# Kernel optimization log

Hardware: AMD Instinct MI355X
Metric: run time of the kernel (lower is better)

The kernel has to match this reference:

```python
import jax, jax.numpy as jnp
import numpy as np

N, E, IN, H, D = 100000, 1600000, 128, 4, 64
NEG_SLOPE = 0.2
K_APPNP, ALPHA = 5, 0.5
BN_EPS = 1e-5


def setup_inputs() -> dict:
    key = jax.random.key(0)
    ks = jax.random.split(key, 12)
    return {
        'node_feats': jax.random.normal(ks[0], (N, IN), jnp.float32),
        'src': jax.random.randint(ks[1], (E,), 0, N, jnp.int32),
        'dst': jax.random.randint(ks[2], (E,), 0, N, jnp.int32),
        'W_fc': jax.random.normal(ks[3], (IN, H * D), jnp.float32) * (1.0 / np.sqrt(IN)),
        'attn_l': jax.random.normal(ks[4], (H, D), jnp.float32) * 0.1,
        'attn_r': jax.random.normal(ks[5], (H, D), jnp.float32) * 0.1,
        'W_res_gat': jax.random.normal(ks[6], (IN, H * D), jnp.float32) * (1.0 / np.sqrt(IN)),
        'gat_bias': jax.random.normal(ks[7], (H * D,), jnp.float32) * 0.01,
        'conv_w': jax.random.normal(ks[8], (1, H), jnp.float32) * 0.5,
        'conv_b': jax.random.normal(ks[9], (1,), jnp.float32) * 0.01,
        'W_res': jax.random.normal(ks[10], (D, IN), jnp.float32) * (1.0 / np.sqrt(IN)),
        'b_res': jax.random.normal(ks[11], (D,), jnp.float32) * 0.01,
        'gamma': jnp.ones((D,), jnp.float32),
        'beta': jnp.zeros((D,), jnp.float32),
    }


def reference(node_feats, src, dst, W_fc, attn_l, attn_r, W_res_gat, gat_bias,
              conv_w, conv_b, W_res, b_res, gamma, beta):
    # ---- GATConv (4 heads, residual, relu) ----
    feat = (node_feats @ W_fc).reshape(N, H, D)            # (N,H,D)
    el = jnp.einsum('nhd,hd->nh', feat, attn_l)            # (N,H)
    er = jnp.einsum('nhd,hd->nh', feat, attn_r)
    e = jax.nn.leaky_relu(el[src] + er[dst], NEG_SLOPE)    # (E,H)
    # edge softmax over incoming edges of each dst node
    emax = jax.ops.segment_max(e, dst, num_segments=N)     # (N,H)
    emax = jnp.where(jnp.isfinite(emax), emax, 0.0)
    ee = jnp.exp(e - emax[dst])                            # (E,H)
    denom = jax.ops.segment_sum(ee, dst, num_segments=N)   # (N,H)
    a = ee / jnp.maximum(denom[dst], 1e-9)                 # (E,H)
    msg = feat[src] * a[..., None]                         # (E,H,D)
    rst = jax.ops.segment_sum(msg, dst, num_segments=N)    # (N,H,D)
    resval = (node_feats @ W_res_gat).reshape(N, H, D)
    rst = jax.nn.relu(rst + resval + gat_bias.reshape(1, H, D))
    # ---- Conv1d (heads -> 1, kernel_size=1) then flatten ----
    h = jnp.einsum('nhd,oh->nod', rst, conv_w) + conv_b[None, :, None]
    h = h.reshape(N, D)
    # ---- APPNP (k=5, alpha=0.5), symmetric deg^{-1/2} norm (in-degree, clamp 1) ----
    deg = jax.ops.segment_sum(jnp.ones((E,), jnp.float32), dst, num_segments=N)
    norm = jnp.power(jnp.maximum(deg, 1.0), -0.5)[:, None]  # (N,1)
    h0 = h
    for _ in range(K_APPNP):
        h = jax.ops.segment_sum((h * norm)[src], dst, num_segments=N) * norm
        h = (1.0 - ALPHA) * h + ALPHA * h0
    # ---- residual linear + relu ----
    h = h + jax.nn.relu(node_feats @ W_res.T + b_res)
    # ---- BatchNorm1d (batch stats, affine) ----
    mu = h.mean(axis=0)
    var = h.var(axis=0)
    return (h - mu) * jax.lax.rsqrt(var + BN_EPS) * gamma + beta
```

## Files before the change

kernel.cpp:

```cpp
#include <hip/hip_runtime.h>
#include <math.h>

#define NN 100000
#define NE 1600000
#define NEG_SLOPE 0.2f

typedef __attribute__((ext_vector_type(8))) short bf16x8;
typedef __attribute__((ext_vector_type(4))) float f32x4;
typedef __attribute__((ext_vector_type(2))) float f32x2;

__device__ __forceinline__ float b2f(unsigned short u) {
  union { unsigned u; float f; } c; c.u = ((unsigned)u) << 16; return c.f;
}
__device__ __forceinline__ unsigned short f2b(float x) {
  union { float f; unsigned u; } c; c.f = x;
  unsigned r = c.u + 0x7FFFu + ((c.u >> 16) & 1u);
  return (unsigned short)(r >> 16);
}
__device__ __forceinline__ void fma4(float4& acc, float s, const float4& b) {
  acc.x = fmaf(s, b.x, acc.x);
  acc.y = fmaf(s, b.y, acc.y);
  acc.z = fmaf(s, b.z, acc.z);
  acc.w = fmaf(s, b.w, acc.w);
}
__device__ __forceinline__ float wred(float v) {
#pragma unroll
  for (int off = 32; off > 0; off >>= 1) v += __shfl_xor(v, off, 64);
  return v;
}

__global__ __launch_bounds__(256) void k_zero(int* __restrict__ p, int nwords) {
  int i = blockIdx.x * 256 + threadIdx.x;
  if (i < nwords) p[i] = 0;
}

__global__ void k_zrow(unsigned short* __restrict__ a, unsigned short* __restrict__ b) {
  int i = threadIdx.x;
  a[(size_t)NN * 64 + i] = 0;
  b[(size_t)NN * 64 + i] = 0;
}

__global__ __launch_bounds__(256) void k_cast(const float* __restrict__ A, unsigned short* __restrict__ Ab) {
  int i = blockIdx.x * 256 + threadIdx.x;
  int i4 = i * 4;
  if (i4 < NN * 128) {
    float4 v = *(const float4*)&A[i4];
    ushort4 o; o.x = f2b(v.x); o.y = f2b(v.y); o.z = f2b(v.z); o.w = f2b(v.w);
    *(ushort4*)&Ab[i4] = o;
  }
}

__global__ __launch_bounds__(256) void k_deg(const int* __restrict__ dst, int* __restrict__ deg) {
  int i = blockIdx.x * 256 + threadIdx.x;
  if (i < NE) atomicAdd(&deg[dst[i]], 1);
}

__global__ __launch_bounds__(256) void k_alloc(const int* __restrict__ deg, int* __restrict__ row_start,
                                               int* __restrict__ counter, float* __restrict__ nrm) {
  int i = blockIdx.x * 256 + threadIdx.x;
  if (i < NN) {
    row_start[i] = atomicAdd(counter, deg[i]);
    nrm[i] = rsqrtf(fmaxf((float)deg[i], 1.0f));
  }
}

__global__ __launch_bounds__(256) void k_scatter(const int* __restrict__ src, const int* __restrict__ dst,
                                                 const int* __restrict__ row_start, int* __restrict__ cursor,
                                                 int* __restrict__ csr_src) {
  int i = blockIdx.x * 256 + threadIdx.x;
  if (i < NE) {
    int n = dst[i];
    int p = atomicAdd(&cursor[n], 1);
    csr_src[row_start[n] + p] = src[i];
  }
}

__global__ __launch_bounds__(256) void k_prepw(const float* __restrict__ W_fc, const float* __restrict__ al,
                                               const float* __restrict__ ar, float* __restrict__ w) {
  int o = blockIdx.x * 256 + threadIdx.x;
  if (o >= 1024) return;
  int side = o >> 9;
  int h = (o >> 7) & 3;
  int k = o & 127;
  const float* a = side ? ar : al;
  float s = 0.f;
  for (int d = 0; d < 64; ++d) s += W_fc[k * 256 + h * 64 + d] * a[h * 64 + d];
  w[(side * 4 + h) * 128 + k] = s;
}

__global__ __launch_bounds__(256) void k_elr2(const float* __restrict__ X, const float* __restrict__ w,
                                              float* __restrict__ el, float* __restrict__ er) {
  int n = blockIdx.x * 32 + (threadIdx.x >> 3);
  int p = threadIdx.x & 7;
  if (n >= NN) return;
  const float4* xr = (const float4*)(X + (size_t)n * 128);
  const float4* wr = (const float4*)(w + p * 128);
  float s = 0.f;
#pragma unroll
  for (int i = 0; i < 32; ++i) {
    float4 x = xr[i], ww = wr[i];
    s += x.x * ww.x + x.y * ww.y + x.z * ww.z + x.w * ww.w;
  }
  if (p < 4) el[n * 4 + p] = s;
  else er[n * 4 + (p - 4)] = s;
}

__global__ __launch_bounds__(256) void k_prepB(const float* __restrict__ W_fc, const float* __restrict__ W_rg,
                                               unsigned short* __restrict__ Bp) {
  int y = blockIdx.y;
  const float* Bsrc = (y >> 1) ? W_rg : W_fc;
  int colbase = (y & 1) * 128;
  for (int e = blockIdx.x * 256 + threadIdx.x; e < 16384; e += 2048) {
    int n = e & 127, k = e >> 7;
    int p = colbase + n;
    int d = p >> 2, hh = p & 3;
    float v = Bsrc[k * 256 + hh * 64 + d];
    int nt = n >> 4, nn = n & 15, kt = k >> 5, quad = (k >> 3) & 3, j = k & 7;
    Bp[(size_t)y * 16384 + ((nt * 4 + kt) * 64 + quad * 16 + nn) * 8 + j] = f2b(v);
  }
}

__global__ __launch_bounds__(256) void k_gemm_mfma(const unsigned short* __restrict__ Abf,
                                                   const unsigned short* __restrict__ Bp,
                                                   unsigned* __restrict__ feat8u,
                                                   unsigned short* __restrict__ resval2) {
  __shared__ unsigned short Bl[16384];
  int tid = threadIdx.x;
  int half = blockIdx.y >> 1;
  int colbase = (blockIdx.y & 1) * 128;
  {
    const uint4* src = (const uint4*)(Bp + (size_t)blockIdx.y * 16384);
    uint4* dst4 = (uint4*)Bl;
#pragma unroll
    for (int i = 0; i < 8; ++i) dst4[tid + i * 256] = src[tid + i * 256];
  }
  __syncthreads();
  int w = tid >> 6, lane = tid & 63;
  int quad = lane >> 4;
  int row0 = blockIdx.x * 128;
  int mrow = row0 + (lane & 15);
  f32x4 acc[8][2];
#pragma unroll
  for (int rt = 0; rt < 8; ++rt)
#pragma unroll
    for (int c = 0; c < 2; ++c) acc[rt][c] = (f32x4){0.f, 0.f, 0.f, 0.f};
#pragma unroll
  for (int kt = 0; kt < 4; ++kt) {
    bf16x8 b0 = *(const bf16x8*)&Bl[(((w * 2 + 0) * 4 + kt) * 64 + lane) * 8];
    bf16x8 b1 = *(const bf16x8*)&Bl[(((w * 2 + 1) * 4 + kt) * 64 + lane) * 8];
    int kb = kt * 32 + quad * 8;
#pragma unroll
    for (int rt = 0; rt < 8; ++rt) {
      int rr = mrow + rt * 16; if (rr > NN - 1) rr = NN - 1;
      bf16x8 a = *(const bf16x8*)&Abf[(size_t)rr * 128 + kb];
      acc[rt][0] = __builtin_amdgcn_mfma_f32_16x16x32_bf16(b0, a, acc[rt][0], 0, 0, 0);
      acc[rt][1] = __builtin_amdgcn_mfma_f32_16x16x32_bf16(b1, a, acc[rt][1], 0, 0, 0);
    }
  }
#pragma unroll
  for (int rt = 0; rt < 8; ++rt) {
    int m = row0 + rt * 16 + (lane & 15);
    if (m < NN) {
#pragma unroll
      for (int c = 0; c < 2; ++c) {
        int col = colbase + (w * 2 + c) * 16 + quad * 4;
        if (half == 0) {
          int pk = __builtin_amdgcn_cvt_pk_fp8_f32(acc[rt][c][0], acc[rt][c][1], 0, false);
          pk = __builtin_amdgcn_cvt_pk_fp8_f32(acc[rt][c][2], acc[rt][c][3], pk, true);
          feat8u[(size_t)m * 64 + (col >> 2)] = (unsigned)pk;
        } else {
          ushort4 o;
          o.x = f2b(acc[rt][c][0]); o.y = f2b(acc[rt][c][1]);
          o.z = f2b(acc[rt][c][2]); o.w = f2b(acc[rt][c][3]);
          *(ushort4*)&resval2[(size_t)m * 256 + col] = o;
        }
      }
    }
  }
}

__global__ __launch_bounds__(256) void k_gemm_nt_bias_relu(const float* __restrict__ A, const float* __restrict__ B,
                                                           const float* __restrict__ bias, float* __restrict__ C) {
  __shared__ float Bl[128][68];
  for (int idx = threadIdx.x; idx < 64 * 128; idx += 256) {
    int d = idx >> 7, k = idx & 127;
    Bl[k][d] = B[d * 128 + k];
  }
  __syncthreads();
  int tx = threadIdx.x & 15, ty = threadIdx.x >> 4;
  int row0 = blockIdx.x * 64 + ty * 4;
  const float* ap[4];
#pragma unroll
  for (int r = 0; r < 4; ++r) ap[r] = A + (size_t)min(row0 + r, NN - 1) * 128;
  float4 acc[4];
#pragma unroll
  for (int r = 0; r < 4; ++r) acc[r] = make_float4(0.f, 0.f, 0.f, 0.f);
#pragma unroll 2
  for (int k0 = 0; k0 < 128; k0 += 4) {
    float4 b0 = *(const float4*)&Bl[k0][tx * 4];
    float4 b1 = *(const float4*)&Bl[k0 + 1][tx * 4];
    float4 b2 = *(const float4*)&Bl[k0 + 2][tx * 4];
    float4 b3 = *(const float4*)&Bl[k0 + 3][tx * 4];
#pragma unroll
    for (int r = 0; r < 4; ++r) {
      float4 a = *(const float4*)(ap[r] + k0);
      fma4(acc[r], a.x, b0); fma4(acc[r], a.y, b1);
      fma4(acc[r], a.z, b2); fma4(acc[r], a.w, b3);
    }
  }
  float4 bv = *(const float4*)&bias[tx * 4];
#pragma unroll
  for (int r = 0; r < 4; ++r) {
    int row = row0 + r;
    if (row < NN) {
      float4 v;
      v.x = fmaxf(acc[r].x + bv.x, 0.f);
      v.y = fmaxf(acc[r].y + bv.y, 0.f);
      v.z = fmaxf(acc[r].z + bv.z, 0.f);
      v.w = fmaxf(acc[r].w + bv.w, 0.f);
      *(float4*)&C[(size_t)row * 64 + tx * 4] = v;
    }
  }
}

__global__ __launch_bounds__(256) void k_gat(const int* __restrict__ row_start, const int* __restrict__ deg,
                                             const int* __restrict__ csr_src, const float* __restrict__ el,
                                             const float* __restrict__ er, const unsigned* __restrict__ feat8u,
                                             const unsigned short* __restrict__ resval2,
                                             const float* __restrict__ gat_bias, const float* __restrict__ conv_w,
                                             const float* __restrict__ conv_b, const float* __restrict__ nrm,
                                             float* __restrict__ h0, unsigned short* __restrict__ hsA) {
  __shared__ int s_src[4][64];
  __shared__ float s_x[4][64][4];
  int wid = threadIdx.x >> 6, lane = threadIdx.x & 63;
  int n = blockIdx.x * 4 + wid;
  if (n >= NN) return;
  int s0 = row_start[n], cnt = deg[n];
  float4 er4 = *(const float4*)&er[n * 4];
  int k = lane & 31, g = lane >> 5;
  unsigned koff = (unsigned)(k << 3);
  f32x2 a01_0 = (f32x2){0.f, 0.f}, a23_0 = (f32x2){0.f, 0.f};
  f32x2 a01_1 = (f32x2){0.f, 0.f}, a23_1 = (f32x2){0.f, 0.f};
  float den0 = 0.f, den1 = 0.f, den2 = 0.f, den3 = 0.f;
  for (int base = 0; base < cnt; base += 64) {
    int j = base + lane;
    int s = 0;
    float x0 = 0.f, x1 = 0.f, x2 = 0.f, x3 = 0.f;
    if (j < cnt) {
      s = csr_src[s0 + j];
      float4 el4 = *(const float4*)&el[s * 4];
      float e0 = el4.x + er4.x; e0 = (e0 > 0.f) ? e0 : NEG_SLOPE * e0;
      float e1 = el4.y + er4.y; e1 = (e1 > 0.f) ? e1 : NEG_SLOPE * e1;
      float e2 = el4.z + er4.z; e2 = (e2 > 0.f) ? e2 : NEG_SLOPE * e2;
      float e3 = el4.w + er4.w; e3 = (e3 > 0.f) ? e3 : NEG_SLOPE * e3;
      x0 = __expf(e0); x1 = __expf(e1); x2 = __expf(e2); x3 = __expf(e3);
      den0 += x0; den1 += x1; den2 += x2; den3 += x3;
    }
    s_src[wid][lane] = s;
    *(float4*)&s_x[wid][lane][0] = make_float4(x0, x1, x2, x3);
    int m = cnt - base; if (m > 64) m = 64;
    int mr = (m + 3) & ~3;
    for (int t = 0; t < mr; t += 4) {
      int sA = s_src[wid][t + g];
      int sB = s_src[wid][t + 2 + g];
      float4 xA = *(const float4*)&s_x[wid][t + g][0];
      float4 xB = *(const float4*)&s_x[wid][t + 2 + g][0];
      uint2 fA = *(const uint2*)((const char*)feat8u + (((unsigned)sA << 8) + koff));
      uint2 fB = *(const uint2*)((const char*)feat8u + (((unsigned)sB << 8) + koff));
      f32x2 xa01 = (f32x2){xA.x, xA.y}, xa23 = (f32x2){xA.z, xA.w};
      f32x2 xb01 = (f32x2){xB.x, xB.y}, xb23 = (f32x2){xB.z, xB.w};
      f32x2 lo, hi;
      lo = __builtin_amdgcn_cvt_pk_f32_fp8((int)fA.x, false);
      hi = __builtin_amdgcn_cvt_pk_f32_fp8((int)fA.x, true);
      a01_0 += xa01 * lo; a23_0 += xa23 * hi;
      lo = __builtin_amdgcn_cvt_pk_f32_fp8((int)fA.y, false);
      hi = __builtin_amdgcn_cvt_pk_f32_fp8((int)fA.y, true);
      a01_1 += xa01 * lo; a23_1 += xa23 * hi;
      lo = __builtin_amdgcn_cvt_pk_f32_fp8((int)fB.x, false);
      hi = __builtin_amdgcn_cvt_pk_f32_fp8((int)fB.x, true);
      a01_0 += xb01 * lo; a23_0 += xb23 * hi;
      lo = __builtin_amdgcn_cvt_pk_f32_fp8((int)fB.y, false);
      hi = __builtin_amdgcn_cvt_pk_f32_fp8((int)fB.y, true);
      a01_1 += xb01 * lo; a23_1 += xb23 * hi;
    }
  }
  den0 = wred(den0); den1 = wred(den1); den2 = wred(den2); den3 = wred(den3);
  float i0 = 1.f / fmaxf(den0, 1e-9f);
  float i1 = 1.f / fmaxf(den1, 1e-9f);
  float i2 = 1.f / fmaxf(den2, 1e-9f);
  float i3 = 1.f / fmaxf(den3, 1e-9f);
  a01_0[0] += __shfl_xor(a01_0[0], 32, 64);
  a01_0[1] += __shfl_xor(a01_0[1], 32, 64);
  a23_0[0] += __shfl_xor(a23_0[0], 32, 64);
  a23_0[1] += __shfl_xor(a23_0[1], 32, 64);
  a01_1[0] += __shfl_xor(a01_1[0], 32, 64);
  a01_1[1] += __shfl_xor(a01_1[1], 32, 64);
  a23_1[0] += __shfl_xor(a23_1[0], 32, 64);
  a23_1[1] += __shfl_xor(a23_1[1], 32, 64);
  if (lane < 32) {
    int d0 = k << 1;
    uint4 rv = *(const uint4*)&resval2[(size_t)n * 256 + ((unsigned)k << 3)];
    float2 bb0 = *(const float2*)&gat_bias[d0];
    float2 bb1 = *(const float2*)&gat_bias[64 + d0];
    float2 bb2 = *(const float2*)&gat_bias[128 + d0];
    float2 bb3 = *(const float2*)&gat_bias[192 + d0];
    float cb = conv_b[0];
    float cw0 = conv_w[0], cw1 = conv_w[1], cw2 = conv_w[2], cw3 = conv_w[3];
    float t, hm0 = cb, hm1 = cb;
    t = fmaf(a01_0[0], i0, b2f((unsigned short)(rv.x & 0xffffu)) + bb0.x); t = fmaxf(t, 0.f); hm0 = fmaf(cw0, t, hm0);
    t = fmaf(a01_0[1], i1, b2f((unsigned short)(rv.x >> 16)) + bb1.x);     t = fmaxf(t, 0.f); hm0 = fmaf(cw1, t, hm0);
    t = fmaf(a23_0[0], i2, b2f((unsigned short)(rv.y & 0xffffu)) + bb2.x); t = fmaxf(t, 0.f); hm0 = fmaf(cw2, t, hm0);
    t = fmaf(a23_0[1], i3, b2f((unsigned short)(rv.y >> 16)) + bb3.x);     t = fmaxf(t, 0.f); hm0 = fmaf(cw3, t, hm0);
    t = fmaf(a01_1[0], i0, b2f((unsigned short)(rv.z & 0xffffu)) + bb0.y); t = fmaxf(t, 0.f); hm1 = fmaf(cw0, t, hm1);
    t = fmaf(a01_1[1], i1, b2f((unsigned short)(rv.z >> 16)) + bb1.y);     t = fmaxf(t, 0.f); hm1 = fmaf(cw1, t, hm1);
    t = fmaf(a23_1[0], i2, b2f((unsigned short)(rv.w & 0xffffu)) + bb2.y); t = fmaxf(t, 0.f); hm1 = fmaf(cw2, t, hm1);
    t = fmaf(a23_1[1], i3, b2f((unsigned short)(rv.w >> 16)) + bb3.y);     t = fmaxf(t, 0.f); hm1 = fmaf(cw3, t, hm1);
    float nn_ = nrm[n];
    size_t o = (size_t)n * 64 + d0;
    *(float2*)&h0[o] = make_float2(hm0, hm1);
    ushort2 hs; hs.x = f2b(hm0 * nn_); hs.y = f2b(hm1 * nn_);
    *(ushort2*)&hsA[o] = hs;
  }
}

__device__ __forceinline__ void gather_accum(const int* __restrict__ row_start, const int* __restrict__ deg,
                                             const int* __restrict__ csr_src,
                                             const unsigned short* __restrict__ hs_in,
                                             int n, int wid, int lane,
                                             float& a0, float& a1, float& a2, float& a3) {
  __shared__ int s_src[4][64];
  int s0 = row_start[n], cnt = deg[n];
  int k = lane & 15, g = lane >> 4;
  unsigned koff = (unsigned)(k << 3);
  a0 = 0.f; a1 = 0.f; a2 = 0.f; a3 = 0.f;
  for (int base = 0; base < cnt; base += 64) {
    int j = base + lane;
    s_src[wid][lane] = (j < cnt) ? csr_src[s0 + j] : NN;
    int m = cnt - base; if (m > 64) m = 64;
    int mr = (m + 7) & ~7;
    for (int t = 0; t < mr; t += 8) {
      int sA = s_src[wid][t + g];
      int sB = s_src[wid][t + 4 + g];
      uint2 uA = *(const uint2*)((const char*)hs_in + (((unsigned)sA << 7) + koff));
      uint2 uB = *(const uint2*)((const char*)hs_in + (((unsigned)sB << 7) + koff));
      a0 += __uint_as_float(uA.x << 16);
      a1 += __uint_as_float(uA.x & 0xFFFF0000u);
      a2 += __uint_as_float(uA.y << 16);
      a3 += __uint_as_float(uA.y & 0xFFFF0000u);
      a0 += __uint_as_float(uB.x << 16);
      a1 += __uint_as_float(uB.x & 0xFFFF0000u);
      a2 += __uint_as_float(uB.y << 16);
      a3 += __uint_as_float(uB.y & 0xFFFF0000u);
    }
  }
  a0 += __shfl_xor(a0, 16, 64); a1 += __shfl_xor(a1, 16, 64);
  a2 += __shfl_xor(a2, 16, 64); a3 += __shfl_xor(a3, 16, 64);
  a0 += __shfl_xor(a0, 32, 64); a1 += __shfl_xor(a1, 32, 64);
  a2 += __shfl_xor(a2, 32, 64); a3 += __shfl_xor(a3, 32, 64);
}

__global__ __launch_bounds__(256) void k_gather_mid(const int* __restrict__ row_start, const int* __restrict__ deg,
                                                    const int* __restrict__ csr_src,
                                                    const unsigned short* __restrict__ hs_in,
                                                    const float* __restrict__ nrm, const float* __restrict__ h0,
                                                    unsigned short* __restrict__ hs_out) {
  int wid = threadIdx.x >> 6, lane = threadIdx.x & 63;
  int n = blockIdx.x * 4 + wid;
  if (n >= NN) return;
  float a0, a1, a2, a3;
  gather_accum(row_start, deg, csr_src, hs_in, n, wid, lane, a0, a1, a2, a3);
  if (lane < 16) {
    size_t o = (size_t)n * 64 + (lane << 2);
    float nn_ = nrm[n];
    float4 h4 = *(const float4*)&h0[o];
    float hn = 0.5f * nn_;
    float v0 = fmaf(hn, a0, 0.5f * h4.x) * nn_;
    float v1 = fmaf(hn, a1, 0.5f * h4.y) * nn_;
    float v2 = fmaf(hn, a2, 0.5f * h4.z) * nn_;
    float v3 = fmaf(hn, a3, 0.5f * h4.w) * nn_;
    ushort4 ov; ov.x = f2b(v0); ov.y = f2b(v1); ov.z = f2b(v2); ov.w = f2b(v3);
    *(ushort4*)&hs_out[o] = ov;
  }
}

__global__ __launch_bounds__(256) void k_gather_last(const int* __restrict__ row_start, const int* __restrict__ deg,
                                                     const int* __restrict__ csr_src,
                                                     const unsigned short* __restrict__ hs_in,
                                                     const float* __restrict__ nrm,
                                                     const float* __restrict__ res2,
                                                     float* h0io) {
  int wid = threadIdx.x >> 6, lane = threadIdx.x & 63;
  int n = blockIdx.x * 4 + wid;
  if (n >= NN) return;
  float a0, a1, a2, a3;
  gather_accum(row_start, deg, csr_src, hs_in, n, wid, lane, a0, a1, a2, a3);
  if (lane < 16) {
    size_t o = (size_t)n * 64 + (lane << 2);
    float nn_ = nrm[n];
    float4 h4 = *(const float4*)&h0io[o];
    float4 r4 = *(const float4*)&res2[o];
    float hn = 0.5f * nn_;
    float4 v;
    v.x = fmaf(hn, a0, 0.5f * h4.x) + r4.x;
    v.y = fmaf(hn, a1, 0.5f * h4.y) + r4.y;
    v.z = fmaf(hn, a2, 0.5f * h4.z) + r4.z;
    v.w = fmaf(hn, a3, 0.5f * h4.w) + r4.w;
    *(float4*)&h0io[o] = v;
  }
}

__global__ __launch_bounds__(256) void k_finred(const float* __restrict__ hfin, float* __restrict__ bn) {
  __shared__ float s1[256], s2[256];
  int d = threadIdx.x & 63;
  int rb = blockIdx.x * 64;
  float sum = 0.f, sq = 0.f;
  for (int r = threadIdx.x >> 6; r < 64; r += 4) {
    int n = rb + r;
    if (n < NN) {
      float v = hfin[(size_t)n * 64 + d];
      sum += v; sq += v * v;
    }
  }
  s1[threadIdx.x] = sum; s2[threadIdx.x] = sq;
  __syncthreads();
  if (threadIdx.x < 128) { s1[threadIdx.x] += s1[threadIdx.x + 128]; s2[threadIdx.x] += s2[threadIdx.x + 128]; }
  __syncthreads();
  if (threadIdx.x < 64) {
    atomicAdd(&bn[d], s1[threadIdx.x] + s1[threadIdx.x + 64]);
    atomicAdd(&bn[64 + d], s2[threadIdx.x] + s2[threadIdx.x + 64]);
  }
}

__global__ void k_bnstats(const float* __restrict__ bn, const float* __restrict__ gamma,
                          const float* __restrict__ beta, float* __restrict__ bns) {
  int d = threadIdx.x;
  float mu = bn[d] * (1.0f / NN);
  float var = fmaxf(bn[64 + d] * (1.0f / NN) - mu * mu, 0.f);
  float sc = rsqrtf(var + 1e-5f) * gamma[d];
  bns[d] = sc;
  bns[64 + d] = beta[d] - mu * sc;
}

__global__ __launch_bounds__(256) void k_bnapply(const float* __restrict__ h, const float* __restrict__ bns,
                                                 float* __restrict__ out) {
  int i = blockIdx.x * 256 + threadIdx.x;
  if (i < NN * 64) {
    int d = i & 63;
    out[i] = fmaf(h[i], bns[d], bns[64 + d]);
  }
}

extern "C" void kernel_launch(void* const* d_in, const int* in_sizes, int n_in,
                              void* d_out, int out_size, void* d_ws, size_t ws_size,
                              hipStream_t stream) {
  const float* node_feats = (const float*)d_in[0];
  const int* src = (const int*)d_in[1];
  const int* dst = (const int*)d_in[2];
  const float* W_fc = (const float*)d_in[3];
  const float* attn_l = (const float*)d_in[4];
  const float* attn_r = (const float*)d_in[5];
  const float* W_res_gat = (const float*)d_in[6];
  const float* gat_bias = (const float*)d_in[7];
  const float* conv_w = (const float*)d_in[8];
  const float* conv_b = (const float*)d_in[9];
  const float* W_res = (const float*)d_in[10];
  const float* b_res = (const float*)d_in[11];
  const float* gamma = (const float*)d_in[12];
  const float* beta = (const float*)d_in[13];
  float* out = (float*)d_out;

  char* base = (char*)d_ws;
  size_t off = 0;
  auto alloc = [&](size_t bytes) -> char* {
    char* p = base + off;
    off = (off + bytes + 255) & ~(size_t)255;
    return p;
  };
  unsigned* feat8u        = (unsigned*)alloc((size_t)NN * 256);
  unsigned short* resval2 = (unsigned short*)alloc((size_t)NN * 256 * 2);
  float* res2             = (float*)resval2;
  float* el               = (float*)alloc((size_t)NN * 4 * 4);
  float* er               = (float*)alloc((size_t)NN * 4 * 4);
  float* h0               = (float*)alloc((size_t)NN * 64 * 4);
  unsigned short* Abf     = (unsigned short*)h0;
  unsigned short* hsA     = (unsigned short*)alloc((size_t)(NN + 1) * 64 * 2);
  unsigned short* hsB     = (unsigned short*)alloc((size_t)(NN + 1) * 64 * 2);
  int* csr_src            = (int*)alloc((size_t)NE * 4);
  float* nrm              = (float*)alloc((size_t)NN * 4);
  int* row_start          = (int*)alloc((size_t)NN * 4);
  unsigned short* Bpacked = (unsigned short*)alloc((size_t)4 * 16384 * 2);
  float* w_elr            = (float*)alloc((size_t)8 * 128 * 4);
  size_t zoff = off;
  int* deg                = (int*)alloc((size_t)NN * 4);
  int* cursor             = (int*)alloc((size_t)NN * 4);
  int* counter            = (int*)alloc(256);
  float* bn               = (float*)alloc(256 * 4);
  float* hfin             = h0;

  int zwords = (int)((off - zoff) / 4);
  int gE = (NE + 255) / 256;
  int gN = (NN + 255) / 256;
  int gW = (NN + 3) / 4;
  int gM = (NN + 63) / 64;
  int gV = (NN * 64 + 255) / 256;

  k_zero<<<(zwords + 255) / 256, 256, 0, stream>>>((int*)(base + zoff), zwords);
  k_zrow<<<1, 64, 0, stream>>>(hsA, hsB);
  k_deg<<<gE, 256, 0, stream>>>(dst, deg);
  k_alloc<<<gN, 256, 0, stream>>>(deg, row_start, counter, nrm);
  k_scatter<<<gE, 256, 0, stream>>>(src, dst, row_start, cursor, csr_src);

  k_cast<<<(NN * 128 / 4 + 255) / 256, 256, 0, stream>>>(node_feats, Abf);
  k_prepB<<<dim3(8, 4), 256, 0, stream>>>(W_fc, W_res_gat, Bpacked);
  k_prepw<<<4, 256, 0, stream>>>(W_fc, attn_l, attn_r, w_elr);
  k_gemm_mfma<<<dim3((NN + 127) / 128, 4), 256, 0, stream>>>(Abf, Bpacked, feat8u, resval2);

  k_elr2<<<(NN + 31) / 32, 256, 0, stream>>>(node_feats, w_elr, el, er);
  k_gat<<<gW, 256, 0, stream>>>(row_start, deg, csr_src, el, er, feat8u, resval2,
                                gat_bias, conv_w, conv_b, nrm, h0, hsA);

  k_gemm_nt_bias_relu<<<gM, 256, 0, stream>>>(node_feats, W_res, b_res, res2);

  k_gather_mid<<<gW, 256, 0, stream>>>(row_start, deg, csr_src, hsA, nrm, h0, hsB);
  k_gather_mid<<<gW, 256, 0, stream>>>(row_start, deg, csr_src, hsB, nrm, h0, hsA);
  k_gather_mid<<<gW, 256, 0, stream>>>(row_start, deg, csr_src, hsA, nrm, h0, hsB);
  k_gather_mid<<<gW, 256, 0, stream>>>(row_start, deg, csr_src, hsB, nrm, h0, hsA);
  k_gather_last<<<gW, 256, 0, stream>>>(row_start, deg, csr_src, hsA, nrm, res2, hfin);

  k_finred<<<gM, 256, 0, stream>>>(hfin, bn);
  k_bnstats<<<1, 64, 0, stream>>>(bn, gamma, beta, bn + 128);
  k_bnapply<<<gV, 256, 0, stream>>>(hfin, bn + 128, out);
}
```

Before: 834.9 us.

## Stage GEMM A tile in LDS, coalesce epilogue stores, fuse softmax denominator

The MFMA GEMM now copies the 128x128 bf16 A tile into padded LDS and loads B in two K halves, so the smaller B buffer makes room in LDS. The epilogue writes its results through LDS and then stores full coalesced 16-byte rows to feat8u and resval2, replacing the scattered 4- and 8-byte global writes. In the GAT kernel, the softmax denominator is now accumulated inside the gather loop from the staged values, which replaces the 6-step wave reduction with a single xor-32 shuffle. The cost is more LDS per block, which may lower occupancy, plus extra barriers.

```diff
diff --git a/kernel.cpp b/kernel.cpp
--- a/kernel.cpp
+++ b/kernel.cpp
@@ -22,11 +22,6 @@
   acc.y = fmaf(s, b.y, acc.y);
   acc.z = fmaf(s, b.z, acc.z);
   acc.w = fmaf(s, b.w, acc.w);
-}
-__device__ __forceinline__ float wred(float v) {
-#pragma unroll
-  for (int off = 32; off > 0; off >>= 1) v += __shfl_xor(v, off, 64);
-  return v;
 }
 
 __global__ __launch_bounds__(256) void k_zero(int* __restrict__ p, int nwords) {
@@ -116,7 +111,7 @@
     int d = p >> 2, hh = p & 3;
     float v = Bsrc[k * 256 + hh * 64 + d];
     int nt = n >> 4, nn = n & 15, kt = k >> 5, quad = (k >> 3) & 3, j = k & 7;
-    Bp[(size_t)y * 16384 + ((nt * 4 + kt) * 64 + quad * 16 + nn) * 8 + j] = f2b(v);
+    Bp[(size_t)y * 16384 + ((kt * 8 + nt) * 64 + quad * 16 + nn) * 8 + j] = f2b(v);
   }
 }
 
@@ -124,57 +119,96 @@
                                                    const unsigned short* __restrict__ Bp,
                                                    unsigned* __restrict__ feat8u,
                                                    unsigned short* __restrict__ resval2) {
-  __shared__ unsigned short Bl[16384];
+  __shared__ unsigned short Al[128 * 136];
+  __shared__ unsigned short Bl[8192];
   int tid = threadIdx.x;
   int half = blockIdx.y >> 1;
   int colbase = (blockIdx.y & 1) * 128;
+  int row0 = blockIdx.x * 128;
+#pragma unroll
+  for (int i = 0; i < 8; ++i) {
+    int c = tid + i * 256;
+    int row = c >> 4, part = c & 15;
+    int gr = row0 + row; if (gr > NN - 1) gr = NN - 1;
+    *(uint4*)&Al[row * 136 + part * 8] = *(const uint4*)&Abf[(size_t)gr * 128 + part * 8];
+  }
   {
-    const uint4* src = (const uint4*)(Bp + (size_t)blockIdx.y * 16384);
+    const uint4* srcb = (const uint4*)(Bp + (size_t)blockIdx.y * 16384);
     uint4* dst4 = (uint4*)Bl;
 #pragma unroll
-    for (int i = 0; i < 8; ++i) dst4[tid + i * 256] = src[tid + i * 256];
+    for (int i = 0; i < 4; ++i) dst4[tid + i * 256] = srcb[tid + i * 256];
   }
   __syncthreads();
   int w = tid >> 6, lane = tid & 63;
-  int quad = lane >> 4;
-  int row0 = blockIdx.x * 128;
-  int mrow = row0 + (lane & 15);
+  int quad = lane >> 4, l16 = lane & 15;
   f32x4 acc[8][2];
 #pragma unroll
   for (int rt = 0; rt < 8; ++rt)
 #pragma unroll
     for (int c = 0; c < 2; ++c) acc[rt][c] = (f32x4){0.f, 0.f, 0.f, 0.f};
 #pragma unroll
-  for (int kt = 0; kt < 4; ++kt) {
-    bf16x8 b0 = *(const bf16x8*)&Bl[(((w * 2 + 0) * 4 + kt) * 64 + lane) * 8];
-    bf16x8 b1 = *(const bf16x8*)&Bl[(((w * 2 + 1) * 4 + kt) * 64 + lane) * 8];
-    int kb = kt * 32 + quad * 8;
-#pragma unroll
-    for (int rt = 0; rt < 8; ++rt) {
-      int rr = mrow + rt * 16; if (rr > NN - 1) rr = NN - 1;
-      bf16x8 a = *(const bf16x8*)&Abf[(size_t)rr * 128 + kb];
-      acc[rt][0] = __builtin_amdgcn_mfma_f32_16x16x32_bf16(b0, a, acc[rt][0], 0, 0, 0);
-      acc[rt][1] = __builtin_amdgcn_mfma_f32_16x16x32_bf16(b1, a, acc[rt][1], 0, 0, 0);
-    }
-  }
-#pragma unroll
-  for (int rt = 0; rt < 8; ++rt) {
-    int m = row0 + rt * 16 + (lane & 15);
-    if (m < NN) {
+  for (int kh = 0; kh < 2; ++kh) {
+    if (kh == 1) {
+      __syncthreads();
+      const uint4* srcb = (const uint4*)(Bp + (size_t)blockIdx.y * 16384 + 8192);
+      uint4* dst4 = (uint4*)Bl;
+#pragma unroll
+      for (int i = 0; i < 4; ++i) dst4[tid + i * 256] = srcb[tid + i * 256];
+      __syncthreads();
+    }
+#pragma unroll
+    for (int ktl = 0; ktl < 2; ++ktl) {
+      int kt = kh * 2 + ktl;
+      bf16x8 b0 = *(const bf16x8*)&Bl[((ktl * 8 + w * 2 + 0) * 64 + lane) * 8];
+      bf16x8 b1 = *(const bf16x8*)&Bl[((ktl * 8 + w * 2 + 1) * 64 + lane) * 8];
+      int kb = kt * 32 + quad * 8;
+#pragma unroll
+      for (int rt = 0; rt < 8; ++rt) {
+        bf16x8 a = *(const bf16x8*)&Al[(rt * 16 + l16) * 136 + kb];
+        acc[rt][0] = __builtin_amdgcn_mfma_f32_16x16x32_bf16(b0, a, acc[rt][0], 0, 0, 0);
+        acc[rt][1] = __builtin_amdgcn_mfma_f32_16x16x32_bf16(b1, a, acc[rt][1], 0, 0, 0);
+      }
+    }
+  }
+  __syncthreads();
+  if (half == 0) {
+    unsigned* Cl = (unsigned*)Al;
+#pragma unroll
+    for (int rt = 0; rt < 8; ++rt)
 #pragma unroll
       for (int c = 0; c < 2; ++c) {
-        int col = colbase + (w * 2 + c) * 16 + quad * 4;
-        if (half == 0) {
-          int pk = __builtin_amdgcn_cvt_pk_fp8_f32(acc[rt][c][0], acc[rt][c][1], 0, false);
-          pk = __builtin_amdgcn_cvt_pk_fp8_f32(acc[rt][c][2], acc[rt][c][3], pk, true);
-          feat8u[(size_t)m * 64 + (col >> 2)] = (unsigned)pk;
-        } else {
-          ushort4 o;
-          o.x = f2b(acc[rt][c][0]); o.y = f2b(acc[rt][c][1]);
-          o.z = f2b(acc[rt][c][2]); o.w = f2b(acc[rt][c][3]);
-          *(ushort4*)&resval2[(size_t)m * 256 + col] = o;
-        }
+        int pk = __builtin_amdgcn_cvt_pk_fp8_f32(acc[rt][c][0], acc[rt][c][1], 0, false);
+        pk = __builtin_amdgcn_cvt_pk_fp8_f32(acc[rt][c][2], acc[rt][c][3], pk, true);
+        Cl[(rt * 16 + l16) * 36 + (w * 2 + c) * 4 + quad] = (unsigned)pk;
       }
+    __syncthreads();
+#pragma unroll
+    for (int i = 0; i < 4; ++i) {
+      int c = tid + i * 256;
+      int row = c >> 3, wp = c & 7;
+      int m = row0 + row;
+      if (m < NN)
+        *(uint4*)&feat8u[(size_t)m * 64 + (colbase >> 2) + wp * 4] = *(const uint4*)&Cl[row * 36 + wp * 4];
+    }
+  } else {
+#pragma unroll
+    for (int rt = 0; rt < 8; ++rt)
+#pragma unroll
+      for (int c = 0; c < 2; ++c) {
+        int col = (w * 2 + c) * 16 + quad * 4;
+        ushort4 o;
+        o.x = f2b(acc[rt][c][0]); o.y = f2b(acc[rt][c][1]);
+        o.z = f2b(acc[rt][c][2]); o.w = f2b(acc[rt][c][3]);
+        *(ushort4*)&Al[(rt * 16 + l16) * 136 + col] = o;
+      }
+    __syncthreads();
+#pragma unroll
+    for (int i = 0; i < 8; ++i) {
+      int c = tid + i * 256;
+      int row = c >> 4, part = c & 15;
+      int m = row0 + row;
+      if (m < NN)
+        *(uint4*)&resval2[(size_t)m * 256 + colbase + part * 8] = *(const uint4*)&Al[row * 136 + part * 8];
     }
   }
 }
@@ -241,7 +275,7 @@
   unsigned koff = (unsigned)(k << 3);
   f32x2 a01_0 = (f32x2){0.f, 0.f}, a23_0 = (f32x2){0.f, 0.f};
   f32x2 a01_1 = (f32x2){0.f, 0.f}, a23_1 = (f32x2){0.f, 0.f};
-  float den0 = 0.f, den1 = 0.f, den2 = 0.f, den3 = 0.f;
+  f32x2 den01 = (f32x2){0.f, 0.f}, den23 = (f32x2){0.f, 0.f};
   for (int base = 0; base < cnt; base += 64) {
     int j = base + lane;
     int s = 0;
@@ -254,7 +288,6 @@
       float e2 = el4.z + er4.z; e2 = (e2 > 0.f) ? e2 : NEG_SLOPE * e2;
       float e3 = el4.w + er4.w; e3 = (e3 > 0.f) ? e3 : NEG_SLOPE * e3;
       x0 = __expf(e0); x1 = __expf(e1); x2 = __expf(e2); x3 = __expf(e3);
-      den0 += x0; den1 += x1; den2 += x2; den3 += x3;
     }
     s_src[wid][lane] = s;
     *(float4*)&s_x[wid][lane][0] = make_float4(x0, x1, x2, x3);
@@ -269,6 +302,8 @@
       uint2 fB = *(const uint2*)((const char*)feat8u + (((unsigned)sB << 8) + koff));
       f32x2 xa01 = (f32x2){xA.x, xA.y}, xa23 = (f32x2){xA.z, xA.w};
       f32x2 xb01 = (f32x2){xB.x, xB.y}, xb23 = (f32x2){xB.z, xB.w};
+      den01 += xa01; den01 += xb01;
+      den23 += xa23; den23 += xb23;
       f32x2 lo, hi;
       lo = __builtin_amdgcn_cvt_pk_f32_fp8((int)fA.x, false);
       hi = __builtin_amdgcn_cvt_pk_f32_fp8((int)fA.x, true);
@@ -284,11 +319,14 @@
       a01_1 += xb01 * lo; a23_1 += xb23 * hi;
     }
   }
-  den0 = wred(den0); den1 = wred(den1); den2 = wred(den2); den3 = wred(den3);
-  float i0 = 1.f / fmaxf(den0, 1e-9f);
-  float i1 = 1.f / fmaxf(den1, 1e-9f);
-  float i2 = 1.f / fmaxf(den2, 1e-9f);
-  float i3 = 1.f / fmaxf(den3, 1e-9f);
+  den01[0] += __shfl_xor(den01[0], 32, 64);
+  den01[1] += __shfl_xor(den01[1], 32, 64);
+  den23[0] += __shfl_xor(den23[0], 32, 64);
+  den23[1] += __shfl_xor(den23[1], 32, 64);
+  float i0 = 1.f / fmaxf(den01[0], 1e-9f);
+  float i1 = 1.f / fmaxf(den01[1], 1e-9f);
+  float i2 = 1.f / fmaxf(den23[0], 1e-9f);
+  float i3 = 1.f / fmaxf(den23[1], 1e-9f);
   a01_0[0] += __shfl_xor(a01_0[0], 32, 64);
   a01_0[1] += __shfl_xor(a01_0[1], 32, 64);
   a23_0[0] += __shfl_xor(a23_0[0], 32, 64);
```

After: 781.4 us. 6.4% less time.
